# Performance work log

Hardware: AMD Instinct MI355X
Metric: run time of the kernel (lower is better)

## Reference

```python
import jax, jax.numpy as jnp
import numpy as np

# ---- constants from init_kwargs ----
PC = (-51.2, -51.2, -5.0, 51.2, 51.2, 3.0)
D = 4          # num_points_in_pillar
ZMAX = 8       # Z default in gen_reference_points
BEV_H = 256; BEV_W = 256
Q = BEV_H * BEV_W
NUMCAM = 6
VBH = 256; VBW = 256
MAXLEN = VBH * VBW
MAX_OVER = 6
IMH, IMW = 512, 928   # data['img'].shape[2:]
EPS = 1e-5


def _gen_ref3d(bs):
    # gen_reference_points(dim='3d'): (bs, D, Q, 3), normalized coords
    zs = jnp.linspace(0.5, ZMAX - 0.5, D) / ZMAX
    xs = jnp.linspace(0.5, BEV_W - 0.5, BEV_W) / BEV_W
    ys = jnp.linspace(0.5, BEV_H - 0.5, BEV_H) / BEV_H
    g = jnp.stack([
        jnp.broadcast_to(xs[None, None, :], (D, BEV_H, BEV_W)),
        jnp.broadcast_to(ys[None, :, None], (D, BEV_H, BEV_W)),
        jnp.broadcast_to(zs[:, None, None], (D, BEV_H, BEV_W)),
    ], -1).reshape(D, Q, 3)
    return jnp.broadcast_to(g[None], (bs, D, Q, 3))


def setup_inputs() -> dict:
    key = jax.random.key(0)
    ego2img = jax.random.normal(key, (4, NUMCAM, 4, 4), dtype=jnp.float32)
    return {"ego2img": ego2img}


def reference(ego2img):
    B = ego2img.shape[0]
    ref = _gen_ref3d(B)                                   # (B,D,Q,3)
    x = ref[..., 0] * (PC[3] - PC[0]) + PC[0]
    y = ref[..., 1] * (PC[4] - PC[1]) + PC[1]
    z = ref[..., 2] * (PC[5] - PC[2]) + PC[2]
    pts = jnp.stack([x, y, z, jnp.ones_like(x)], -1)      # (B,D,Q,4) homogeneous

    # project each pillar point through each camera matrix
    cam = jnp.einsum('bcij,bdqj->bcdqi', ego2img, pts)    # (B,C,D,Q,4)
    zc = cam[..., 2]
    uv = cam[..., 0:2] / jnp.maximum(zc, EPS)[..., None]
    u = uv[..., 0] / IMW
    v = uv[..., 1] / IMH
    vis = (zc > EPS) & (v > 0.0) & (v < 1.0) & (u < 1.0) & (u > 0.0)  # (B,C,D,Q)
    rpc = jnp.clip(jnp.stack([u, v], -1), -2.1, 2.1)       # (B,C,D,Q,2)

    ref_cam = jnp.transpose(rpc, (1, 0, 3, 2, 4))          # (C,B,Q,D,2)
    vis_any = jnp.any(jnp.transpose(vis, (1, 0, 3, 2)), -1)  # (C,B,Q) pillar visible in cam

    qidx = jnp.arange(Q)
    qx = qidx % BEV_W
    qy = qidx // BEV_W
    # normalized BEV coords of each pillar (align_corners=True convention)
    gxy = jnp.stack([qx / (BEV_W - 1.0), qy / (BEV_H - 1.0)], -1) * 2.0 - 1.0

    # ---- queries_rebatch_grid: pack visible pillar coords densely per camera ----
    vis_bc = jnp.transpose(vis_any, (1, 0, 2)).reshape(B * NUMCAM, Q)

    def make_grid(vrow):
        rank = jnp.cumsum(vrow.astype(jnp.int32)) - 1      # position among visible pillars
        pos = jnp.where(vrow, rank, MAXLEN)                # invisible -> dummy slot
        buf = jnp.full((MAXLEN + 1, 2), -1.5, dtype=jnp.float32)
        return buf.at[pos].set(gxy)[:MAXLEN]

    grids = jax.vmap(make_grid)(vis_bc)                    # (B*C, MAXLEN, 2)
    queries_rebatch_grid = grids.reshape(B * NUMCAM, VBH, VBW, 2)

    # ---- reference_points_rebatch: grid_sample(nearest, align_corners=True, zeros pad) ----
    src = jnp.transpose(ref_cam.reshape(NUMCAM, B, Q, D * 2), (1, 0, 3, 2))
    src = src.reshape(B * NUMCAM, D * 2, Q)               # (B*C, D*2, H*W)
    ix = jnp.round((grids[..., 0] + 1.0) * 0.5 * (BEV_W - 1)).astype(jnp.int32)
    iy = jnp.round((grids[..., 1] + 1.0) * 0.5 * (BEV_H - 1)).astype(jnp.int32)
    ok = (ix >= 0) & (ix < BEV_W) & (iy >= 0) & (iy < BEV_H)
    gq = jnp.clip(iy * BEV_W + ix, 0, Q - 1)              # (B*C, MAXLEN)
    gathered = jnp.take_along_axis(src, gq[:, None, :], axis=2) * ok[:, None, :]
    reference_points_rebatch = jnp.transpose(gathered, (0, 2, 1)).reshape(
        B * NUMCAM, MAXLEN, D, 2)

    # ---- restore_bev_grid: map each (camera, pillar) slot back to dense BEV rows ----
    RB = MAX_OVER * BEV_H * BEV_W
    cam_off = jnp.arange(NUMCAM)[:, None] * VBH

    def make_restore(vis_b):  # (C, Q) bool
        vi = vis_b.astype(jnp.int32)
        rank = jnp.cumsum(vi, axis=1) - 1                  # packed index inside camera
        over = jnp.cumsum(vi, axis=0) - vi                 # overlap slot (exclusive count)
        gx = (rank % VBW) / (VBW - 1.0) * 2.0 - 1.0
        gy = (cam_off + rank // VBW) / (NUMCAM * VBH - 1.0) * 2.0 - 1.0
        flat = (over * BEV_H + qy[None]) * BEV_W + qx[None]
        flat = jnp.where(vis_b & (over < MAX_OVER), flat, RB)
        buf = jnp.full((RB + 1, 2), -1.5, dtype=jnp.float32)
        buf = buf.at[flat.reshape(-1)].set(jnp.stack([gx, gy], -1).reshape(-1, 2))
        return buf[:RB].reshape(MAX_OVER * BEV_H, BEV_W, 2)

    restore_bev_grid = jax.vmap(make_restore)(jnp.transpose(vis_any, (1, 0, 2)))

    # ---- bev_pillar_counts: 1 / (#cameras seeing each pillar) ----
    count = jnp.sum(vis_any.astype(jnp.float32), axis=0)   # (B, Q)
    bev_pillar_counts = (1.0 / jnp.maximum(count, 1.0))[..., None]

    return (queries_rebatch_grid, restore_bev_grid,
            reference_points_rebatch, bev_pillar_counts)
```

## Files before the change

kernel.cpp:

```cpp
#include <hip/hip_runtime.h>

#define NCAM      6
#define NB        4
#define NROWS     24
#define NQ        65536
#define MAXLEN_   65536

#define OFF_QGRID   0
#define OFF_RESTORE 3145728
#define OFF_REFPTS  6291456
#define OFF_COUNTS  18874368

__device__ __forceinline__ float zval(int d) {
    const float z[4] = { -4.5f, -2.16666674613952637f,
                          0.166666507720947266f, 2.5f };
    return z[d];
}

__device__ __forceinline__ float clip21(float x) {
    return fminf(fmaxf(x, -2.1f), 2.1f);
}

__device__ __forceinline__ bool proj_point(const float m[12], float x, float y, float z,
                                           float& u, float& v) {
    float c0 = ((m[0]*x + m[1]*y) + m[2]*z) + m[3];
    float c1 = ((m[4]*x + m[5]*y) + m[6]*z) + m[7];
    float c2 = ((m[8]*x + m[9]*y) + m[10]*z) + m[11];
    float zcl = fmaxf(c2, 1e-5f);
    float inv = __builtin_amdgcn_rcpf(zcl);
    u = (c0 * inv) * (1.0f / 928.0f);
    v = (c1 * inv) * (1.0f / 512.0f);
    return (c2 > 1e-5f) & (c1 > 0.0f) & (c1 < 512.0f * zcl)
         & (c0 > 0.0f) & (c0 < 928.0f * zcl);
}

__device__ __forceinline__ void load_mat(const float* __restrict__ ego2img, int row, float m[12]) {
    const float* M = ego2img + row * 16;
    #pragma unroll
    for (int i = 0; i < 12; ++i) m[i] = M[i];
}

__device__ __forceinline__ void bev_xy(int qx, int qy, float& x, float& y) {
    x = ((float)qx + 0.5f) * (1.0f/256.0f) * 102.4f - 51.2f;
    y = ((float)qy + 0.5f) * (1.0f/256.0f) * 102.4f - 51.2f;
}

__global__ void __launch_bounds__(256)
k_count(const float* __restrict__ ego2img, int* __restrict__ chunkCounts)
{
    int chunk = blockIdx.x, row = blockIdx.y;
    float m[12]; load_mat(ego2img, row, m);
    int t = threadIdx.x;
    int lane = t & 63;
    int q0 = chunk * 1024 + t * 4;
    int cnt = 0;
    #pragma unroll
    for (int i = 0; i < 4; ++i) {
        int q = q0 + i;
        float x, y; bev_xy(q & 255, q >> 8, x, y);
        bool va = false;
        #pragma unroll
        for (int d = 0; d < 4; ++d) {
            float u, v;
            va |= proj_point(m, x, y, zval(d), u, v);
        }
        unsigned long long bal = __ballot(va);
        if (lane == 0) cnt += __popcll(bal);
    }
    if (lane == 0)
        chunkCounts[row * 256 + chunk * 4 + (t >> 6)] = cnt;
}

__global__ void __launch_bounds__(384)
k_fused(const float* __restrict__ ego2img, const int* __restrict__ chunkCounts,
        float* __restrict__ out)
{
    int chunk = blockIdx.x, b = blockIdx.y;
    int t = threadIdx.x;
    int lane = t & 63;
    int c = t >> 6;
    unsigned long long lt = (1ull << lane) - 1ull;

    __shared__ int lrank[NCAM][256];

    int row = __builtin_amdgcn_readfirstlane(b * NCAM + c);

    const int* p = chunkCounts + row * 256;
    int4 v4 = ((const int4*)p)[lane];
    int s = v4.x + v4.y + v4.z + v4.w;
    int incl = s;
    #pragma unroll
    for (int off = 1; off < 64; off <<= 1) {
        int nn = __shfl_up(incl, off, 64);
        if (lane >= off) incl += nn;
    }
    int k = chunk & 3;
    int bb = incl - s + ((k > 0) ? v4.x : 0)
                      + ((k > 1) ? v4.y : 0)
                      + ((k > 2) ? v4.z : 0);
    int base  = __shfl(bb,   chunk >> 2, 64);
    int total = __shfl(incl, 63,        64);

    float m[12]; load_mat(ego2img, row, m);

    float2* qgrid  = (float2*)(out + OFF_QGRID)  + (size_t)row * MAXLEN_;
    float4* refpF4 = (float4*)(out + OFF_REFPTS) + (size_t)row * (MAXLEN_ * 2);

    int qy = chunk;

    #pragma unroll
    for (int i = 0; i < 4; ++i) {
        int qx = i * 64 + lane;
        float x, y; bev_xy(qx, qy, x, y);
        float uv[8];
        bool vis = false;
        #pragma unroll
        for (int d = 0; d < 4; ++d) {
            float u, v;
            bool vi = proj_point(m, x, y, zval(d), u, v);
            uv[2*d]   = clip21(u);
            uv[2*d+1] = clip21(v);
            vis |= vi;
        }
        unsigned long long bal = __ballot(vis);
        int r = base + __popcll(bal & lt);
        if (vis) {
            float2 g;
            g.x = ((float)qx / 255.0f) * 2.0f - 1.0f;
            g.y = ((float)qy / 255.0f) * 2.0f - 1.0f;
            qgrid[r] = g;
            refpF4[2*r]     = make_float4(uv[0], uv[1], uv[2], uv[3]);
            refpF4[2*r + 1] = make_float4(uv[4], uv[5], uv[6], uv[7]);
        }
        lrank[c][qx] = vis ? r : -1;
        base += __popcll(bal);
    }

    int s0 = max(total, chunk << 8);
    int n  = ((chunk + 1) << 8) - s0;
    if (n > 0) {
        for (int j = lane; j < n; j += 64)
            qgrid[s0 + j] = make_float2(-1.5f, -1.5f);
        float4 z4 = make_float4(0.f, 0.f, 0.f, 0.f);
        for (int j = lane; j < 2 * n; j += 64)
            refpF4[2*s0 + j] = z4;
    }

    __syncthreads();

    float2* rest = (float2*)(out + OFF_RESTORE) + (size_t)b * NCAM * NQ;
    int o = c;
    #pragma unroll
    for (int i = 0; i < 4; ++i) {
        int qx = i * 64 + lane;
        float2 val = make_float2(-1.5f, -1.5f);
        int cnt = 0;
        #pragma unroll
        for (int cc = 0; cc < NCAM; ++cc) {
            int r = lrank[cc][qx];
            bool v = (r >= 0);
            if (v && (cnt == o)) {
                val.x = ((float)(r & 255) / 255.0f) * 2.0f - 1.0f;
                val.y = ((float)(cc * 256 + (r >> 8)) / 1535.0f) * 2.0f - 1.0f;
            }
            cnt += v;
        }
        rest[(o * 256 + qy) * 256 + qx] = val;
        if (c == 0)
            out[OFF_COUNTS + (size_t)b * NQ + qy * 256 + qx] =
                1.0f / fmaxf((float)cnt, 1.0f);
    }
}

extern "C" void kernel_launch(void* const* d_in, const int* in_sizes, int n_in,
                              void* d_out, int out_size, void* d_ws, size_t ws_size,
                              hipStream_t stream)
{
    const float* ego2img = (const float*)d_in[0];
    float* out = (float*)d_out;
    int* chunkCounts = (int*)d_ws;

    k_count<<<dim3(64, NROWS), 256, 0, stream>>>(ego2img, chunkCounts);
    k_fused<<<dim3(256, NB),   384, 0, stream>>>(ego2img, chunkCounts, out);
}
```

Measured before the change: 90.48 us.

## Merge count and fused kernels into one cooperative kernel with grid sync

Replaces the two-kernel launch (count pass, then fused pack/restore pass) with a single cooperative kernel that runs the count phase, performs a grid-wide sync, then runs the fused phase. The count work is redistributed so each wave handles one 256-query chunk of one camera row. This removes a kernel launch and the inter-kernel gap, at the cost of a grid barrier and a requirement that all 1024 blocks of 384 threads be co-resident. If the cooperative launch fails, it falls back to the original two kernels.

```diff
diff --git a/kernel.cpp b/kernel.cpp
--- a/kernel.cpp
+++ b/kernel.cpp
@@ -1,4 +1,7 @@
 #include <hip/hip_runtime.h>
+#include <hip/hip_cooperative_groups.h>
+
+namespace cg = cooperative_groups;
 
 #define NCAM      6
 #define NB        4
@@ -45,14 +48,13 @@
     y = ((float)qy + 0.5f) * (1.0f/256.0f) * 102.4f - 51.2f;
 }
 
-__global__ void __launch_bounds__(256)
-k_count(const float* __restrict__ ego2img, int* __restrict__ chunkCounts)
-{
-    int chunk = blockIdx.x, row = blockIdx.y;
+__device__ __forceinline__ void count_phase(const float* __restrict__ ego2img,
+                                            int* __restrict__ chunkCounts, int s)
+{
+    int row = s >> 8, ch = s & 255;
     float m[12]; load_mat(ego2img, row, m);
-    int t = threadIdx.x;
-    int lane = t & 63;
-    int q0 = chunk * 1024 + t * 4;
+    int lane = threadIdx.x & 63;
+    int q0 = ch * 256 + lane * 4;
     int cnt = 0;
     #pragma unroll
     for (int i = 0; i < 4; ++i) {
@@ -68,14 +70,14 @@
         if (lane == 0) cnt += __popcll(bal);
     }
     if (lane == 0)
-        chunkCounts[row * 256 + chunk * 4 + (t >> 6)] = cnt;
-}
-
-__global__ void __launch_bounds__(384)
-k_fused(const float* __restrict__ ego2img, const int* __restrict__ chunkCounts,
-        float* __restrict__ out)
-{
-    int chunk = blockIdx.x, b = blockIdx.y;
+        chunkCounts[row * 256 + ch] = cnt;
+}
+
+__device__ __forceinline__ void fused_phase(const float* __restrict__ ego2img,
+                                            const int* __restrict__ chunkCounts,
+                                            float* __restrict__ out,
+                                            int chunk, int b)
+{
     int t = threadIdx.x;
     int lane = t & 63;
     int c = t >> 6;
@@ -172,6 +174,53 @@
     }
 }
 
+__global__ void __launch_bounds__(384, 6)
+k_all(const float* __restrict__ ego2img, int* __restrict__ chunkCounts,
+      float* __restrict__ out)
+{
+    int bx = blockIdx.x, by = blockIdx.y;
+    int c = threadIdx.x >> 6;
+    int s = ((by << 8) | bx) * NCAM + c;
+    count_phase(ego2img, chunkCounts, s);
+
+    cg::this_grid().sync();
+
+    fused_phase(ego2img, chunkCounts, out, bx, by);
+}
+
+__global__ void __launch_bounds__(256)
+k_count(const float* __restrict__ ego2img, int* __restrict__ chunkCounts)
+{
+    int chunk = blockIdx.x, row = blockIdx.y;
+    float m[12]; load_mat(ego2img, row, m);
+    int t = threadIdx.x;
+    int lane = t & 63;
+    int q0 = chunk * 1024 + t * 4;
+    int cnt = 0;
+    #pragma unroll
+    for (int i = 0; i < 4; ++i) {
+        int q = q0 + i;
+        float x, y; bev_xy(q & 255, q >> 8, x, y);
+        bool va = false;
+        #pragma unroll
+        for (int d = 0; d < 4; ++d) {
+            float u, v;
+            va |= proj_point(m, x, y, zval(d), u, v);
+        }
+        unsigned long long bal = __ballot(va);
+        if (lane == 0) cnt += __popcll(bal);
+    }
+    if (lane == 0)
+        chunkCounts[row * 256 + chunk * 4 + (t >> 6)] = cnt;
+}
+
+__global__ void __launch_bounds__(384)
+k_fused(const float* __restrict__ ego2img, const int* __restrict__ chunkCounts,
+        float* __restrict__ out)
+{
+    fused_phase(ego2img, chunkCounts, out, blockIdx.x, blockIdx.y);
+}
+
 extern "C" void kernel_launch(void* const* d_in, const int* in_sizes, int n_in,
                               void* d_out, int out_size, void* d_ws, size_t ws_size,
                               hipStream_t stream)
@@ -180,6 +229,12 @@
     float* out = (float*)d_out;
     int* chunkCounts = (int*)d_ws;
 
-    k_count<<<dim3(64, NROWS), 256, 0, stream>>>(ego2img, chunkCounts);
-    k_fused<<<dim3(256, NB),   384, 0, stream>>>(ego2img, chunkCounts, out);
-}
+    void* args[3] = { (void*)&ego2img, (void*)&chunkCounts, (void*)&out };
+    hipError_t e = hipLaunchCooperativeKernel((const void*)k_all,
+                                              dim3(256, NB), dim3(384, 1, 1),
+                                              args, 0, stream);
+    if (e != hipSuccess) {
+        k_count<<<dim3(64, NROWS), 256, 0, stream>>>(ego2img, chunkCounts);
+        k_fused<<<dim3(256, NB),   384, 0, stream>>>(ego2img, chunkCounts, out);
+    }
+}
```

Measured after the change: 142.0 us. 56.9% more time.
